# Optimization experiments

Hardware: AMD Instinct MI355X
Metric: run time of the kernel (lower is better)

Reference implementation:

```python
import jax, jax.numpy as jnp
import numpy as np

B, N, D, P, H = 16, 1024, 512, 512, 8
E = P // H  # head dim = 64


def layer_norm(x, g, b, eps=1e-5):
    mu = jnp.mean(x, axis=-1, keepdims=True)
    var = jnp.var(x, axis=-1, keepdims=True)
    return (x - mu) * jax.lax.rsqrt(var + eps) * g + b


def setup_inputs() -> dict:
    key = jax.random.key(0)
    ks = jax.random.split(key, 12)
    s = 0.02
    inp = {
        "x": jax.random.normal(ks[0], (B, N, D), dtype=jnp.float32),
        "Wq": jax.random.normal(ks[1], (D, P), dtype=jnp.float32) * s,
        "bq": jnp.zeros((P,), jnp.float32),
        "Wk": jax.random.normal(ks[2], (D, P), dtype=jnp.float32) * s,
        "bk": jnp.zeros((P,), jnp.float32),
        "Wv": jax.random.normal(ks[3], (D, P), dtype=jnp.float32) * s,
        "bv": jnp.zeros((P,), jnp.float32),
        "Wo": jax.random.normal(ks[4], (P, D), dtype=jnp.float32) * s,
        "bo": jnp.zeros((D,), jnp.float32),
        "ln1_g": jnp.ones((D,), jnp.float32),
        "ln1_b": jnp.zeros((D,), jnp.float32),
        "W1": jax.random.normal(ks[5], (D, 4 * D), dtype=jnp.float32) * s,
        "b1": jnp.zeros((4 * D,), jnp.float32),
        "W2": jax.random.normal(ks[6], (4 * D, D), dtype=jnp.float32) * s,
        "b2": jnp.zeros((D,), jnp.float32),
        "ln2_g": jnp.ones((D,), jnp.float32),
        "ln2_b": jnp.zeros((D,), jnp.float32),
    }
    return inp


def reference(x, Wq, bq, Wk, bk, Wv, bv, Wo, bo, ln1_g, ln1_b, W1, b1, W2, b2, ln2_g, ln2_b):
    # dropout layers are identity in eval mode
    q = (x @ Wq + bq).reshape(B, N, H, E)
    k = (x @ Wk + bk).reshape(B, N, H, E)
    v = (x @ Wv + bv).reshape(B, N, H, E)
    scale = 1.0 / jnp.sqrt(jnp.float32(E))
    scores = jnp.einsum('blhe,bshe->bhls', q, k)  # [B,H,L,S]
    A = jax.nn.softmax(scale * scores, axis=-1)
    V = jnp.einsum('bhls,bshd->blhd', A, v).reshape(B, N, P)
    att = V @ Wo + bo
    x1 = layer_norm(x + att, ln1_g, ln1_b)
    # FFN: 1x1 convs over channel dim == per-token linears, exact GELU
    ff = jax.nn.gelu(x1 @ W1 + b1, approximate=False) @ W2 + b2
    return layer_norm(x1 + ff, ln2_g, ln2_b)
```

## Files before the change

kernel.cpp:

```cpp
#include <hip/hip_runtime.h>
#include <hip/hip_bf16.h>

typedef __hip_bfloat16 bf16;
typedef __bf16 bf16x8 __attribute__((ext_vector_type(8)));
typedef __bf16 bf16x4 __attribute__((ext_vector_type(4)));
typedef float f32x4 __attribute__((ext_vector_type(4)));

static __device__ __forceinline__ f32x4 mfma16(bf16x8 a, bf16x8 b, f32x4 c) {
  return __builtin_amdgcn_mfma_f32_16x16x32_bf16(a, b, c, 0, 0, 0);
}
static __device__ __forceinline__ bf16x8 ld8(const bf16* p) {
  return *reinterpret_cast<const bf16x8*>(p);
}
static __device__ __forceinline__ float toF(float v) { return v; }
static __device__ __forceinline__ float toF(bf16 v) { return __bfloat162float(v); }
static __device__ __forceinline__ void stF(float* p, float v) { *p = v; }
static __device__ __forceinline__ void stF(bf16* p, float v) { *p = __float2bfloat16(v); }

typedef __attribute__((address_space(1))) void gvoid;
typedef __attribute__((address_space(3))) void lvoid;
static __device__ __forceinline__ void gl2lds16(const bf16* g, bf16* l) {
  __builtin_amdgcn_global_load_lds((gvoid*)g, (lvoid*)l, 16, 0, 0);
}

__global__ __launch_bounds__(256) void cvt_kernel(const float* __restrict__ in,
                                                  bf16* __restrict__ out) {
  long i = (long)blockIdx.x * 256 + threadIdx.x;
  float4 v = reinterpret_cast<const float4*>(in)[i];
  bf16x4 o;
  o[0] = __float2bfloat16(v.x); o[1] = __float2bfloat16(v.y);
  o[2] = __float2bfloat16(v.z); o[3] = __float2bfloat16(v.w);
  reinterpret_cast<bf16x4*>(out)[i] = o;
}

__global__ void prep_weights(const float* __restrict__ Wq, const float* __restrict__ Wk,
                             const float* __restrict__ Wv, const float* __restrict__ Wo,
                             const float* __restrict__ W1, const float* __restrict__ W2,
                             bf16* __restrict__ Wtqkv, bf16* __restrict__ WtO,
                             bf16* __restrict__ Wt1, bf16* __restrict__ Wt2) {
  int id = blockIdx.x;
  const float* in;
  bf16* out;
  int K, N, n0, k0;
  if (id < 1024) {
    int which = id >> 8, t = id & 255;
    K = 512; N = 512;
    n0 = (t & 15) * 32; k0 = (t >> 4) * 32;
    if (which == 0)      { in = Wq; out = Wtqkv; }
    else if (which == 1) { in = Wk; out = Wtqkv + (size_t)512 * 512; }
    else if (which == 2) { in = Wv; out = Wtqkv + (size_t)1024 * 512; }
    else                 { in = Wo; out = WtO; }
  } else if (id < 2048) {
    int t = id - 1024;
    in = W1; out = Wt1; K = 512; N = 2048;
    n0 = (t & 63) * 32; k0 = (t >> 6) * 32;
  } else {
    int t = id - 2048;
    in = W2; out = Wt2; K = 2048; N = 512;
    n0 = (t & 15) * 32; k0 = (t >> 4) * 32;
  }
  __shared__ float tile[32][33];
  int tx = threadIdx.x, ty = threadIdx.y;
#pragma unroll
  for (int j = 0; j < 32; j += 8)
    tile[ty + j][tx] = in[(long)(k0 + ty + j) * N + n0 + tx];
  __syncthreads();
#pragma unroll
  for (int j = 0; j < 32; j += 8)
    out[(long)(n0 + ty + j) * K + k0 + tx] = __float2bfloat16(tile[tx][ty + j]);
}

template <int MODE>
__global__ __launch_bounds__(256) void gemm_kernel(
    const bf16* __restrict__ A, const bf16* __restrict__ Wt,
    const float* __restrict__ b0, const float* __restrict__ b1_,
    const float* __restrict__ b2_, bf16* C0, bf16* C1, bf16* C2,
    int K, int ldc, int mmask, int mshift) {
  __shared__ alignas(16) bf16 As[2][128 * 32];
  __shared__ alignas(16) bf16 Bs[2][128 * 32];
  const int tid = threadIdx.x;
  const int wave = tid >> 6, lane = tid & 63;
  const int lr = lane & 15, lq = lane >> 4;
  const int L = blockIdx.x;
  const int m0 = (L & mmask) * 128, n0 = (L >> mshift) * 128;
  const int wm = (wave >> 1) * 64, wn = (wave & 1) * 64;

  const int srow0 = (wave * 2) * 16 + (lane >> 2);
  const int srow1 = (wave * 2 + 1) * 16 + (lane >> 2);
  const int scol = (lane & 3) * 8;
  const bf16* Ag0 = A + (long)(m0 + srow0) * K + scol;
  const bf16* Ag1 = A + (long)(m0 + srow1) * K + scol;
  const bf16* Bg0 = Wt + (long)(n0 + srow0) * K + scol;
  const bf16* Bg1 = Wt + (long)(n0 + srow1) * K + scol;
  const int so0 = (wave * 2) * 16 * 32;
  const int so1 = (wave * 2 + 1) * 16 * 32;

  f32x4 acc[4][4] = {};

  gl2lds16(Ag0, &As[0][so0]);
  gl2lds16(Ag1, &As[0][so1]);
  gl2lds16(Bg0, &Bs[0][so0]);
  gl2lds16(Bg1, &Bs[0][so1]);
  __syncthreads();

  int p = 0;
  for (int k0 = 0; k0 < K; k0 += 32) {
    int kn = k0 + 32;
    if (kn < K) {
      gl2lds16(Ag0 + kn, &As[p ^ 1][so0]);
      gl2lds16(Ag1 + kn, &As[p ^ 1][so1]);
      gl2lds16(Bg0 + kn, &Bs[p ^ 1][so0]);
      gl2lds16(Bg1 + kn, &Bs[p ^ 1][so1]);
    }
    bf16x8 af[4], bfr[4];
#pragma unroll
    for (int i = 0; i < 4; ++i) af[i] = ld8(&As[p][(wm + i * 16 + lr) * 32 + lq * 8]);
#pragma unroll
    for (int j = 0; j < 4; ++j) bfr[j] = ld8(&Bs[p][(wn + j * 16 + lr) * 32 + lq * 8]);
#pragma unroll
    for (int i = 0; i < 4; ++i)
#pragma unroll
      for (int j = 0; j < 4; ++j) acc[i][j] = mfma16(af[i], bfr[j], acc[i][j]);
    __syncthreads();
    p ^= 1;
  }

  const float* bias = b0;
  bf16* C = C0;
  int cb = n0;
  bool vmode = false;
  if (MODE == 2) {
    if (n0 >= 1024)     { bias = b2_; C = C2; cb = n0 - 1024; vmode = true; }
    else if (n0 >= 512) { bias = b1_; C = C1; cb = n0 - 512; }
  }

#pragma unroll
  for (int i = 0; i < 4; ++i) {
#pragma unroll
    for (int j = 0; j < 4; ++j) {
      int col = cb + wn + j * 16 + lr;
      float bv = bias[col];
#pragma unroll
      for (int rr = 0; rr < 4; ++rr) {
        int row = m0 + wm + i * 16 + lq * 4 + rr;
        float v = acc[i][j][rr] + bv;
        if (MODE == 1) v = 0.5f * v * (1.0f + erff(v * 0.70710678118654752f));
        if (MODE == 2 && vmode) {
          int hh = col >> 6, e = col & 63;
          int bb = row >> 10, tok = row & 1023;
          C[(((long)((bb * 8 + hh) * 64 + e)) << 10) + tok] = __float2bfloat16(v);
        } else {
          C[(long)row * ldc + col] = __float2bfloat16(v);
        }
      }
    }
  }
}

__global__ __launch_bounds__(256) void attn_kernel(
    const bf16* Q, const bf16* __restrict__ Km,
    const bf16* __restrict__ Vt, bf16* O) {
  constexpr int SP = 72;
  __shared__ alignas(16) bf16 Pall[4][64 * SP];
  const int tid = threadIdx.x;
  const int wave = tid >> 6, lane = tid & 63;
  const int lr = lane & 15, lq = lane >> 4;
  const int L = blockIdx.x;
  const int bh = ((L >> 5) << 3) | (L & 7);
  const int qc = (L >> 3) & 3;
  const int h = bh & 7, b = bh >> 3;
  const int q0 = qc * 256 + wave * 64;
  bf16* P = Pall[wave];
  const float Cc = 0.18033688011112042f;

  bf16x8 qf[4][2];
#pragma unroll
  for (int qs = 0; qs < 4; ++qs) {
    const bf16* qrow = Q + (long)(b * 1024 + q0 + qs * 16 + lr) * 512 + h * 64;
    qf[qs][0] = ld8(qrow + lq * 8);
    qf[qs][1] = ld8(qrow + 32 + lq * 8);
  }
  const bf16* kbase = Km + (long)(b * 1024) * 512 + h * 64;
  const bf16* vbase = Vt + (long)((b * 8 + h) * 64) * 1024;

  f32x4 oacc[4][4] = {};
  float l_part[4] = {};

  for (int kb = 0; kb < 16; ++kb) {
#pragma unroll
    for (int kt = 0; kt < 4; ++kt) {
      const bf16* krow = kbase + (long)(kb * 64 + kt * 16 + lr) * 512;
      bf16x8 kf0 = ld8(krow + lq * 8);
      bf16x8 kf1 = ld8(krow + 32 + lq * 8);
#pragma unroll
      for (int qs = 0; qs < 4; ++qs) {
        f32x4 t = {};
        t = mfma16(kf0, qf[qs][0], t);
        t = mfma16(kf1, qf[qs][1], t);
        bf16x4 pk;
        float sum = 0.f;
#pragma unroll
        for (int rr = 0; rr < 4; ++rr) {
          float p = exp2f(t[rr] * Cc);
          sum += p;
          pk[rr] = __float2bfloat16(p);
        }
        l_part[qs] += sum;
        *reinterpret_cast<bf16x4*>(&P[(qs * 16 + lr) * SP + kt * 16 + lq * 4]) = pk;
      }
    }
    __builtin_amdgcn_sched_barrier(0);
    bf16x8 pf[4][2];
#pragma unroll
    for (int qs = 0; qs < 4; ++qs) {
      pf[qs][0] = ld8(&P[(qs * 16 + lr) * SP + lq * 8]);
      pf[qs][1] = ld8(&P[(qs * 16 + lr) * SP + 32 + lq * 8]);
    }
#pragma unroll
    for (int j0 = 0; j0 < 4; ++j0) {
      const bf16* vrow = vbase + (long)(j0 * 16 + lr) * 1024 + kb * 64;
      bf16x8 vf0 = ld8(vrow + lq * 8);
      bf16x8 vf1 = ld8(vrow + 32 + lq * 8);
#pragma unroll
      for (int qs = 0; qs < 4; ++qs) {
        oacc[qs][j0] = mfma16(pf[qs][0], vf0, oacc[qs][j0]);
        oacc[qs][j0] = mfma16(pf[qs][1], vf1, oacc[qs][j0]);
      }
    }
    __builtin_amdgcn_sched_barrier(0);
  }

  float linv[4];
#pragma unroll
  for (int qs = 0; qs < 4; ++qs) {
    float l = l_part[qs];
    l += __shfl_xor(l, 16);
    l += __shfl_xor(l, 32);
    linv[qs] = 1.0f / l;
  }
#pragma unroll
  for (int qs = 0; qs < 4; ++qs) {
#pragma unroll
    for (int rr = 0; rr < 4; ++rr) {
      float lv = __shfl(linv[qs], lq * 4 + rr);
#pragma unroll
      for (int j0 = 0; j0 < 4; ++j0)
        O[(long)(b * 1024 + q0 + qs * 16 + lq * 4 + rr) * 512 + h * 64 + j0 * 16 + lr] =
            __float2bfloat16(oacc[qs][j0][rr] * lv);
    }
  }
}

template <typename TX, typename TO>
__global__ __launch_bounds__(256) void add_ln_kernel(
    const TX* __restrict__ X, const bf16* __restrict__ Y,
    const float* __restrict__ g, const float* __restrict__ bb,
    TO* __restrict__ out) {
  const int row = blockIdx.x, t = threadIdx.x;
  __shared__ float s1[4], s2[4];
  long base = (long)row * 512;
  float v0 = toF(X[base + t]) + toF(Y[base + t]);
  float v1 = toF(X[base + 256 + t]) + toF(Y[base + 256 + t]);
  float s = v0 + v1, q = v0 * v0 + v1 * v1;
#pragma unroll
  for (int o = 32; o > 0; o >>= 1) {
    s += __shfl_down(s, o);
    q += __shfl_down(q, o);
  }
  int wv = t >> 6;
  if ((t & 63) == 0) { s1[wv] = s; s2[wv] = q; }
  __syncthreads();
  float St = s1[0] + s1[1] + s1[2] + s1[3];
  float Qt = s2[0] + s2[1] + s2[2] + s2[3];
  float mean = St * (1.f / 512.f);
  float var = Qt * (1.f / 512.f) - mean * mean;
  float rs = rsqrtf(var + 1e-5f);
  stF(&out[base + t], (v0 - mean) * rs * g[t] + bb[t]);
  stF(&out[base + 256 + t], (v1 - mean) * rs * g[256 + t] + bb[256 + t]);
}

extern "C" void kernel_launch(void* const* d_in, const int* in_sizes, int n_in,
                              void* d_out, int out_size, void* d_ws, size_t ws_size,
                              hipStream_t stream) {
  const float* x    = (const float*)d_in[0];
  const float* Wq   = (const float*)d_in[1];
  const float* bq   = (const float*)d_in[2];
  const float* Wk   = (const float*)d_in[3];
  const float* bk   = (const float*)d_in[4];
  const float* Wv   = (const float*)d_in[5];
  const float* bv   = (const float*)d_in[6];
  const float* Wo   = (const float*)d_in[7];
  const float* bo   = (const float*)d_in[8];
  const float* ln1g = (const float*)d_in[9];
  const float* ln1b = (const float*)d_in[10];
  const float* W1   = (const float*)d_in[11];
  const float* b1   = (const float*)d_in[12];
  const float* W2   = (const float*)d_in[13];
  const float* b2   = (const float*)d_in[14];
  const float* ln2g = (const float*)d_in[15];
  const float* ln2b = (const float*)d_in[16];
  float* out = (float*)d_out;

  char* ws = (char*)d_ws;
  size_t off = 0;
  auto alloc = [&](size_t bytes) {
    char* p = ws + off;
    off += (bytes + 255) & ~(size_t)255;
    return (bf16*)p;
  };
  bf16* Wtqkv = alloc((size_t)1536 * 512 * 2);
  bf16* WtO   = alloc((size_t)512 * 512 * 2);
  bf16* Wt1   = alloc((size_t)512 * 2048 * 2);
  bf16* Wt2   = alloc((size_t)2048 * 512 * 2);
  const size_t SB = (size_t)16384 * 512 * 2;

  dim3 tb(32, 8);
  const bool big = ws_size >= (size_t)(112) * 1024 * 1024;

  if (big) {
    bf16* kb  = alloc(SB);
    bf16* xb  = alloc(SB);
    bf16* qb  = alloc(SB);
    bf16* vtb = alloc(SB);
    bf16* sp  = alloc(SB);
    bf16* fb  = alloc(SB);
    bf16* ff1 = xb;
    (void)sp;

    cvt_kernel<<<8192, 256, 0, stream>>>(x, xb);
    prep_weights<<<3072, tb, 0, stream>>>(Wq, Wk, Wv, Wo, W1, W2,
                                          Wtqkv, WtO, Wt1, Wt2);

    gemm_kernel<2><<<1536, 256, 0, stream>>>(xb, Wtqkv, bq, bk, bv,
                                             qb, kb, vtb, 512, 512, 127, 7);
    attn_kernel<<<512, 256, 0, stream>>>(qb, kb, vtb, qb);
    gemm_kernel<0><<<512, 256, 0, stream>>>(qb, WtO, bo, nullptr, nullptr,
                                            vtb, nullptr, nullptr, 512, 512, 127, 7);
    add_ln_kernel<bf16, bf16><<<16384, 256, 0, stream>>>(xb, vtb, ln1g, ln1b, kb);
    gemm_kernel<1><<<2048, 256, 0, stream>>>(kb, Wt1, b1, nullptr, nullptr,
                                             ff1, nullptr, nullptr, 512, 2048, 127, 7);
    gemm_kernel<0><<<512, 256, 0, stream>>>(ff1, Wt2, b2, nullptr, nullptr,
                                            fb, nullptr, nullptr, 2048, 512, 127, 7);
    add_ln_kernel<bf16, float><<<16384, 256, 0, stream>>>(kb, fb, ln2g, ln2b, out);
  } else {
    bf16* xb  = alloc(SB);
    bf16* kb  = alloc(SB);
    bf16* qb  = alloc(SB);
    bf16* vtb = alloc(SB);
    bf16* fb  = alloc(SB / 2);
    bf16* ff1 = qb;

    cvt_kernel<<<8192, 256, 0, stream>>>(x, xb);
    prep_weights<<<3072, tb, 0, stream>>>(Wq, Wk, Wv, Wo, W1, W2,
                                          Wtqkv, WtO, Wt1, Wt2);

    gemm_kernel<2><<<1536, 256, 0, stream>>>(xb, Wtqkv, bq, bk, bv,
                                             qb, kb, vtb, 512, 512, 127, 7);
    attn_kernel<<<512, 256, 0, stream>>>(qb, kb, vtb, qb);
    gemm_kernel<0><<<512, 256, 0, stream>>>(qb, WtO, bo, nullptr, nullptr,
                                            vtb, nullptr, nullptr, 512, 512, 127, 7);
    add_ln_kernel<bf16, bf16><<<16384, 256, 0, stream>>>(xb, vtb, ln1g, ln1b, kb);

    for (int hh = 0; hh < 2; ++hh) {
      const bf16* x1h = kb + (size_t)hh * 8192 * 512;
      gemm_kernel<1><<<1024, 256, 0, stream>>>(x1h, Wt1, b1, nullptr, nullptr,
                                               ff1, nullptr, nullptr, 512, 2048, 63, 6);
      gemm_kernel<0><<<256, 256, 0, stream>>>(ff1, Wt2, b2, nullptr, nullptr,
                                              fb, nullptr, nullptr, 2048, 512, 63, 6);
      add_ln_kernel<bf16, float><<<8192, 256, 0, stream>>>(x1h, fb, ln2g, ln2b,
                                                           out + (size_t)hh * 8192 * 512);
    }
  }
}
```

Before: 404.9 us.

## Split attention over key halves with combine kernel and MFMA row sums

Adds a split-K attention kernel that launches twice as many blocks, each covering half the keys and writing unnormalized partial outputs plus row sums, followed by a combine kernel that adds the halves and normalizes. Row-sum accumulation moves from scalar adds plus cross-lane shuffles to an extra MFMA against a vector of ones, in both attention kernels. The large-workspace threshold is lowered and buffers reassigned so more configurations take the split path. The aim is better occupancy of the GPU with 512 attention blocks, at the cost of extra global traffic for the partials and an additional kernel launch.

After: 404.1 us. No clear change (-0.2%).

```diff
diff --git a/kernel.cpp b/kernel.cpp
--- a/kernel.cpp
+++ b/kernel.cpp
@@ -157,6 +157,121 @@
   }
 }
 
+__global__ __launch_bounds__(256) void attn_splitk(
+    const bf16* __restrict__ Q, const bf16* __restrict__ Km,
+    const bf16* __restrict__ Vt, bf16* __restrict__ Op,
+    float* __restrict__ lsum) {
+  constexpr int SP = 72;
+  __shared__ alignas(16) bf16 Pall[4][64 * SP];
+  const int tid = threadIdx.x;
+  const int wave = tid >> 6, lane = tid & 63;
+  const int lr = lane & 15, lq = lane >> 4;
+  const int L = blockIdx.x;
+  const int bh = ((L >> 6) << 3) | (L & 7);
+  const int qh = (L >> 3) & 7;
+  const int qc = qh & 3, half = qh >> 2;
+  const int h = bh & 7, b = bh >> 3;
+  const int q0 = qc * 256 + wave * 64;
+  bf16* P = Pall[wave];
+  const float Cc = 0.18033688011112042f;
+
+  bf16x8 qf[4][2];
+#pragma unroll
+  for (int qs = 0; qs < 4; ++qs) {
+    const bf16* qrow = Q + (long)(b * 1024 + q0 + qs * 16 + lr) * 512 + h * 64;
+    qf[qs][0] = ld8(qrow + lq * 8);
+    qf[qs][1] = ld8(qrow + 32 + lq * 8);
+  }
+  const bf16* kbase = Km + (long)(b * 1024 + half * 512) * 512 + h * 64;
+  const bf16* vbase = Vt + (long)((b * 8 + h) * 64) * 1024 + half * 512;
+
+  bf16x8 ones;
+#pragma unroll
+  for (int k = 0; k < 8; ++k) ones[k] = __float2bfloat16(1.0f);
+
+  f32x4 oacc[4][4] = {};
+  f32x4 lacc[4] = {};
+
+  for (int kb = 0; kb < 8; ++kb) {
+#pragma unroll
+    for (int kt = 0; kt < 4; ++kt) {
+      const bf16* krow = kbase + (long)(kb * 64 + kt * 16 + lr) * 512;
+      bf16x8 kf0 = ld8(krow + lq * 8);
+      bf16x8 kf1 = ld8(krow + 32 + lq * 8);
+#pragma unroll
+      for (int qs = 0; qs < 4; ++qs) {
+        f32x4 t = {};
+        t = mfma16(kf0, qf[qs][0], t);
+        t = mfma16(kf1, qf[qs][1], t);
+        bf16x4 pk;
+#pragma unroll
+        for (int rr = 0; rr < 4; ++rr) pk[rr] = __float2bfloat16(exp2f(t[rr] * Cc));
+        *reinterpret_cast<bf16x4*>(&P[(qs * 16 + lr) * SP + kt * 16 + lq * 4]) = pk;
+      }
+    }
+    __builtin_amdgcn_sched_barrier(0);
+    bf16x8 pf[4][2];
+#pragma unroll
+    for (int qs = 0; qs < 4; ++qs) {
+      pf[qs][0] = ld8(&P[(qs * 16 + lr) * SP + lq * 8]);
+      pf[qs][1] = ld8(&P[(qs * 16 + lr) * SP + 32 + lq * 8]);
+    }
+#pragma unroll
+    for (int qs = 0; qs < 4; ++qs) {
+      lacc[qs] = mfma16(pf[qs][0], ones, lacc[qs]);
+      lacc[qs] = mfma16(pf[qs][1], ones, lacc[qs]);
+    }
+#pragma unroll
+    for (int j0 = 0; j0 < 4; ++j0) {
+      const bf16* vrow = vbase + (long)(j0 * 16 + lr) * 1024 + kb * 64;
+      bf16x8 vf0 = ld8(vrow + lq * 8);
+      bf16x8 vf1 = ld8(vrow + 32 + lq * 8);
+#pragma unroll
+      for (int qs = 0; qs < 4; ++qs) {
+        oacc[qs][j0] = mfma16(pf[qs][0], vf0, oacc[qs][j0]);
+        oacc[qs][j0] = mfma16(pf[qs][1], vf1, oacc[qs][j0]);
+      }
+    }
+    __builtin_amdgcn_sched_barrier(0);
+  }
+
+  bf16* Oh = Op + (size_t)half * ((size_t)16384 * 512);
+#pragma unroll
+  for (int qs = 0; qs < 4; ++qs)
+#pragma unroll
+    for (int rr = 0; rr < 4; ++rr)
+#pragma unroll
+      for (int j0 = 0; j0 < 4; ++j0)
+        Oh[(long)(b * 1024 + q0 + qs * 16 + lq * 4 + rr) * 512 + h * 64 + j0 * 16 + lr] =
+            __float2bfloat16(oacc[qs][j0][rr]);
+  if (lr == 0) {
+    float* lp = lsum + (size_t)half * 131072 + ((size_t)(b * 8 + h) << 10);
+#pragma unroll
+    for (int qs = 0; qs < 4; ++qs)
+#pragma unroll
+      for (int rr = 0; rr < 4; ++rr)
+        lp[q0 + qs * 16 + lq * 4 + rr] = lacc[qs][rr];
+  }
+}
+
+__global__ __launch_bounds__(256) void attn_combine(
+    const bf16* __restrict__ Op, const float* __restrict__ lsum,
+    bf16* __restrict__ O) {
+  long i = (long)blockIdx.x * 256 + threadIdx.x;
+  long idx = i * 8;
+  int tok = (int)(idx >> 9), col = (int)(idx & 511);
+  int b = tok >> 10, q = tok & 1023, h = col >> 6;
+  int li = (b * 8 + h) * 1024 + q;
+  float inv = 1.0f / (lsum[li] + lsum[131072 + li]);
+  bf16x8 a = ld8(Op + idx);
+  bf16x8 c = ld8(Op + (size_t)16384 * 512 + idx);
+  bf16x8 o;
+#pragma unroll
+  for (int k = 0; k < 8; ++k)
+    o[k] = __float2bfloat16(((float)a[k] + (float)c[k]) * inv);
+  *reinterpret_cast<bf16x8*>(O + idx) = o;
+}
+
 __global__ __launch_bounds__(256) void attn_kernel(
     const bf16* Q, const bf16* __restrict__ Km,
     const bf16* __restrict__ Vt, bf16* O) {
@@ -183,8 +298,12 @@
   const bf16* kbase = Km + (long)(b * 1024) * 512 + h * 64;
   const bf16* vbase = Vt + (long)((b * 8 + h) * 64) * 1024;
 
+  bf16x8 ones;
+#pragma unroll
+  for (int k = 0; k < 8; ++k) ones[k] = __float2bfloat16(1.0f);
+
   f32x4 oacc[4][4] = {};
-  float l_part[4] = {};
+  f32x4 lacc[4] = {};
 
   for (int kb = 0; kb < 16; ++kb) {
 #pragma unroll
@@ -198,14 +317,8 @@
         t = mfma16(kf0, qf[qs][0], t);
         t = mfma16(kf1, qf[qs][1], t);
         bf16x4 pk;
-        float sum = 0.f;
-#pragma unroll
-        for (int rr = 0; rr < 4; ++rr) {
-          float p = exp2f(t[rr] * Cc);
-          sum += p;
-          pk[rr] = __float2bfloat16(p);
-        }
-        l_part[qs] += sum;
+#pragma unroll
+        for (int rr = 0; rr < 4; ++rr) pk[rr] = __float2bfloat16(exp2f(t[rr] * Cc));
         *reinterpret_cast<bf16x4*>(&P[(qs * 16 + lr) * SP + kt * 16 + lq * 4]) = pk;
       }
     }
@@ -215,6 +328,11 @@
     for (int qs = 0; qs < 4; ++qs) {
       pf[qs][0] = ld8(&P[(qs * 16 + lr) * SP + lq * 8]);
       pf[qs][1] = ld8(&P[(qs * 16 + lr) * SP + 32 + lq * 8]);
+    }
+#pragma unroll
+    for (int qs = 0; qs < 4; ++qs) {
+      lacc[qs] = mfma16(pf[qs][0], ones, lacc[qs]);
+      lacc[qs] = mfma16(pf[qs][1], ones, lacc[qs]);
     }
 #pragma unroll
     for (int j0 = 0; j0 < 4; ++j0) {
@@ -230,25 +348,16 @@
     __builtin_amdgcn_sched_barrier(0);
   }
 
-  float linv[4];
-#pragma unroll
-  for (int qs = 0; qs < 4; ++qs) {
-    float l = l_part[qs];
-    l += __shfl_xor(l, 16);
-    l += __shfl_xor(l, 32);
-    linv[qs] = 1.0f / l;
-  }
-#pragma unroll
-  for (int qs = 0; qs < 4; ++qs) {
+#pragma unroll
+  for (int qs = 0; qs < 4; ++qs)
 #pragma unroll
     for (int rr = 0; rr < 4; ++rr) {
-      float lv = __shfl(linv[qs], lq * 4 + rr);
+      float lv = 1.0f / lacc[qs][rr];
 #pragma unroll
       for (int j0 = 0; j0 < 4; ++j0)
         O[(long)(b * 1024 + q0 + qs * 16 + lq * 4 + rr) * 512 + h * 64 + j0 * 16 + lr] =
             __float2bfloat16(oacc[qs][j0][rr] * lv);
     }
-  }
 }
 
 template <typename TX, typename TO>
@@ -315,33 +424,34 @@
   const size_t SB = (size_t)16384 * 512 * 2;
 
   dim3 tb(32, 8);
-  const bool big = ws_size >= (size_t)(112) * 1024 * 1024;
-
-  if (big) {
+
+  if (ws_size >= (size_t)104 * 1024 * 1024) {
+    bf16* xb  = alloc(SB);
     bf16* kb  = alloc(SB);
-    bf16* xb  = alloc(SB);
     bf16* qb  = alloc(SB);
     bf16* vtb = alloc(SB);
-    bf16* sp  = alloc(SB);
-    bf16* fb  = alloc(SB);
-    bf16* ff1 = xb;
-    (void)sp;
+    bf16* p0  = alloc(SB);
+    bf16* p1  = alloc(SB);
+    float* lsum = (float*)alloc((size_t)2 * 131072 * 4);
+    bf16* ff1 = qb;
+    bf16* ff2 = xb;
+    (void)p1;
 
     cvt_kernel<<<8192, 256, 0, stream>>>(x, xb);
     prep_weights<<<3072, tb, 0, stream>>>(Wq, Wk, Wv, Wo, W1, W2,
                                           Wtqkv, WtO, Wt1, Wt2);
-
     gemm_kernel<2><<<1536, 256, 0, stream>>>(xb, Wtqkv, bq, bk, bv,
                                              qb, kb, vtb, 512, 512, 127, 7);
-    attn_kernel<<<512, 256, 0, stream>>>(qb, kb, vtb, qb);
+    attn_splitk<<<1024, 256, 0, stream>>>(qb, kb, vtb, p0, lsum);
+    attn_combine<<<4096, 256, 0, stream>>>(p0, lsum, qb);
     gemm_kernel<0><<<512, 256, 0, stream>>>(qb, WtO, bo, nullptr, nullptr,
                                             vtb, nullptr, nullptr, 512, 512, 127, 7);
     add_ln_kernel<bf16, bf16><<<16384, 256, 0, stream>>>(xb, vtb, ln1g, ln1b, kb);
     gemm_kernel<1><<<2048, 256, 0, stream>>>(kb, Wt1, b1, nullptr, nullptr,
                                              ff1, nullptr, nullptr, 512, 2048, 127, 7);
     gemm_kernel<0><<<512, 256, 0, stream>>>(ff1, Wt2, b2, nullptr, nullptr,
-                                            fb, nullptr, nullptr, 2048, 512, 127, 7);
-    add_ln_kernel<bf16, float><<<16384, 256, 0, stream>>>(kb, fb, ln2g, ln2b, out);
+                                            ff2, nullptr, nullptr, 2048, 512, 127, 7);
+    add_ln_kernel<bf16, float><<<16384, 256, 0, stream>>>(kb, ff2, ln2g, ln2b, out);
   } else {
     bf16* xb  = alloc(SB);
     bf16* kb  = alloc(SB);
@@ -353,7 +463,6 @@
     cvt_kernel<<<8192, 256, 0, stream>>>(x, xb);
     prep_weights<<<3072, tb, 0, stream>>>(Wq, Wk, Wv, Wo, W1, W2,
                                           Wtqkv, WtO, Wt1, Wt2);
-
     gemm_kernel<2><<<1536, 256, 0, stream>>>(xb, Wtqkv, bq, bk, bv,
                                              qb, kb, vtb, 512, 512, 127, 7);
     attn_kernel<<<512, 256, 0, stream>>>(qb, kb, vtb, qb);
```
